# Kernel tuning notes

Measured on AMD Instinct MI355X. Metric: run time of the kernel, lower is better.

## Reference

```python
import jax, jax.numpy as jnp
import numpy as np

# Wrapped Conv2D config (channels_last): input 32x32x32 -> output 32x32x64, 3x3 'same', stride 1
H, W, C_IN, C_OUT = 32, 32, 32, 64


def _propagate(w, b, kernel, bias):
    # w: [B, H*W*C_OUT, n_out], b: [B, n_out]
    B, _, n_out = w.shape
    # transpose(0,2,1) + reshape to [B, n_out, H, W, C_OUT]
    wt = jnp.transpose(w, (0, 2, 1)).reshape(B, n_out, H, W, C_OUT)
    # bias-sum reduction: sum over (h, w, c) of w * bias[c], added to b
    b_new = jnp.einsum('bnhwc,c->bn', wt, bias) + b
    # Batched transposed conv over all n_out slices at once (replaces K.rnn loop)
    z = wt.reshape(B * n_out, H, W, C_OUT)
    w_in = jax.lax.conv_transpose(
        z, kernel, strides=(1, 1), padding='SAME',
        dimension_numbers=('NHWC', 'HWIO', 'NHWC'), transpose_kernel=True)
    # -> [B*n_out, H, W, C_IN]; flatten and transpose back to [B, n_in, n_out]
    w_new = jnp.transpose(w_in.reshape(B, n_out, H * W * C_IN), (0, 2, 1))
    return w_new, b_new


def setup_inputs() -> dict:
    key = jax.random.key(0)
    ks = jax.random.split(key, 6)
    B, n_out = 8, 32
    n_flat = H * W * C_OUT
    return {
        'w_out_u': jax.random.normal(ks[0], (B, n_flat, n_out), jnp.float32),
        'b_out_u': jax.random.normal(ks[1], (B, n_out), jnp.float32),
        'w_out_l': jax.random.normal(ks[2], (B, n_flat, n_out), jnp.float32),
        'b_out_l': jax.random.normal(ks[3], (B, n_out), jnp.float32),
        'kernel': jax.random.normal(ks[4], (3, 3, C_IN, C_OUT), jnp.float32) * 0.1,
        'bias': jax.random.normal(ks[5], (C_OUT,), jnp.float32) * 0.1,
    }


def reference(w_out_u, b_out_u, w_out_l, b_out_l, kernel, bias):
    w_u, b_u = _propagate(w_out_u, b_out_u, kernel, bias)
    w_l, b_l = _propagate(w_out_l, b_out_l, kernel, bias)
    return (w_u, b_u, w_l, b_l)
```

## Files before the change

### kernel.cpp

```cpp
#include <hip/hip_runtime.h>
#include <hip/hip_bf16.h>

#define H  32
#define W  32
#define CI 32
#define CO 64
#define NB 8
#define NOUT 32

#define WU_OFF 0
#define BU_OFF (NB * H * W * CI * NOUT)
#define WL_OFF (BU_OFF + NB * NOUT)
#define BL_OFF (WL_OFF + NB * H * W * CI * NOUT)

#define KF_UINT4 2304
#define BP_OFF_BYTES 36864

typedef __bf16 bf16x8 __attribute__((ext_vector_type(8)));
typedef float  f32x4  __attribute__((ext_vector_type(4)));

__device__ __forceinline__ unsigned int pack_bf16(float lo, float hi) {
    unsigned int ulo = __float_as_uint(lo) + 0x8000u;
    unsigned int uhi = __float_as_uint(hi) + 0x8000u;
    return (uhi & 0xffff0000u) | (ulo >> 16);
}

__global__ void prep_kernel(const float* __restrict__ K,
                            unsigned int* __restrict__ kws,
                            float* __restrict__ bp) {
    int bx = blockIdx.x, t = threadIdx.x;
    if (bx < 9) {
        int g    = bx * 256 + t;
        int tap  = g >> 8;
        int r    = g & 255;
        int i    = r >> 3;
        int og   = r & 7;
        int c    = og >> 2;
        int quad = og & 3;
        int ih   = i >> 4;
        int lane = quad * 16 + (i & 15);
        int dst  = ((tap * 4 + c * 2 + ih) * 64 + lane) * 4;
        const float4* src = (const float4*)(K + (size_t)g * 8);
        float4 f0 = src[0];
        float4 f1 = src[1];
        kws[dst + 0] = pack_bf16(f0.x, f0.y);
        kws[dst + 1] = pack_bf16(f0.z, f0.w);
        kws[dst + 2] = pack_bf16(f1.x, f1.y);
        kws[dst + 3] = pack_bf16(f1.z, f1.w);
    } else {
        bp[(bx - 9) * 256 + t] = 0.f;
    }
}

__global__ __launch_bounds__(512, 4)
void fused_conv_kernel(const float* __restrict__ in0,
                       const float* __restrict__ in1,
                       const uint4* __restrict__ kws,
                       const float* __restrict__ bias,
                       float* __restrict__ bp,
                       float* __restrict__ out0,
                       float* __restrict__ out1) {
    __shared__ uint4 stg[30 * 128];
    __shared__ float bias_s[CO];
    __shared__ float bsum[8][32];

    int t = threadIdx.x;
    if (t < CO) bias_s[t] = bias[t];

    int bx    = blockIdx.x;
    int x     = bx & 7;
    int q     = bx >> 3;
    int combo = x * 2 + (q >> 7);
    int idx   = q & 127;
    int side  = combo >> 3;
    int b     = combo & 7;
    int h     = idx >> 2;
    int wq    = idx & 3;

    const float* inp = (side ? in1 : in0) + (size_t)b * 1024 * 2048;
    const bf16x8* kfp = (const bf16x8*)kws;

    int unit = t >> 5;
    int ogp  = (t >> 3) & 3;
    int n4   = t & 7;
    int wave = t >> 6;
    int lane = t & 63;
    int n16  = lane & 15;
    int quad = lane >> 4;
    int w    = wq * 8 + wave;

    f32x4 acc[2][2] = {};
    float sb[4] = {0.f, 0.f, 0.f, 0.f};
    int rbase = quad * 32 + ((n16 ^ (n16 >> 2)) ^ quad);

    __syncthreads();

    for (int c = 0; c < 2; c++) {
        bf16x8 a[9][2];
#pragma unroll
        for (int tap = 0; tap < 9; tap++) {
            a[tap][0] = kfp[(tap * 4 + c * 2 + 0) * 64 + lane];
            a[tap][1] = kfp[(tap * 4 + c * 2 + 1) * 64 + lane];
        }
#pragma unroll
        for (int s = 0; s < 2; s++) {
            int tile = s * 16 + unit;
            if (tile < 30) {
                int row = tile >= 20 ? 2 : (tile >= 10 ? 1 : 0);
                int col = tile - row * 10;
                int hi  = h - 1 + row;
                int wi  = wq * 8 - 1 + col;
                if (hi >= 0 && hi < H && wi >= 0 && wi < W) {
                    const float* p = inp + (size_t)(hi * W + wi) * 2048
                                   + c * 1024 + ogp * 256 + n4 * 4;
                    float v[8][4];
#pragma unroll
                    for (int j = 0; j < 8; j++) {
                        float4 f = *(const float4*)(p + j * 32);
                        v[j][0] = f.x; v[j][1] = f.y; v[j][2] = f.z; v[j][3] = f.w;
                    }
                    if (row == 1 && col >= 1 && col <= 8) {
#pragma unroll
                        for (int j = 0; j < 8; j++) {
                            float bj = bias_s[c * 32 + ogp * 8 + j];
#pragma unroll
                            for (int k = 0; k < 4; k++)
                                sb[k] = fmaf(v[j][k], bj, sb[k]);
                        }
                    }
                    uint4* dst = &stg[tile * 128 + ogp * 32];
#pragma unroll
                    for (int k = 0; k < 4; k++) {
                        uint4 u;
                        u.x = pack_bf16(v[0][k], v[1][k]);
                        u.y = pack_bf16(v[2][k], v[3][k]);
                        u.z = pack_bf16(v[4][k], v[5][k]);
                        u.w = pack_bf16(v[6][k], v[7][k]);
                        int n = n4 * 4 + k;
                        dst[(n ^ (n >> 2)) ^ ogp] = u;
                    }
                }
            }
        }
        __syncthreads();
        __builtin_amdgcn_s_setprio(1);
#pragma unroll
        for (int kh = 0; kh < 3; kh++) {
            int hi = h + 1 - kh;
            if (hi < 0 || hi >= H) continue;
            int row = 2 - kh;
#pragma unroll
            for (int kw = 0; kw < 3; kw++) {
                int wi = w + 1 - kw;
                if (wi < 0 || wi >= W) continue;
                int col = wave + 2 - kw;
                int tap = kh * 3 + kw;
                const uint4* Tp = &stg[(row * 10 + col) * 128];
                union { uint4 u; bf16x8 v; } b0, b1;
                b0.u = Tp[rbase];
                b1.u = Tp[rbase ^ 20];
                acc[0][0] = __builtin_amdgcn_mfma_f32_16x16x32_bf16(a[tap][0], b0.v, acc[0][0], 0, 0, 0);
                acc[0][1] = __builtin_amdgcn_mfma_f32_16x16x32_bf16(a[tap][0], b1.v, acc[0][1], 0, 0, 0);
                acc[1][0] = __builtin_amdgcn_mfma_f32_16x16x32_bf16(a[tap][1], b0.v, acc[1][0], 0, 0, 0);
                acc[1][1] = __builtin_amdgcn_mfma_f32_16x16x32_bf16(a[tap][1], b1.v, acc[1][1], 0, 0, 0);
            }
        }
        __builtin_amdgcn_s_setprio(0);
        if (c == 0) __syncthreads();
    }

#pragma unroll
    for (int off = 8; off <= 32; off <<= 1)
#pragma unroll
        for (int k = 0; k < 4; k++)
            sb[k] += __shfl_xor(sb[k], off, 64);
    if (lane < 8) {
#pragma unroll
        for (int k = 0; k < 4; k++)
            bsum[wave][lane * 4 + k] = sb[k];
    }
    __syncthreads();
    if (t < 32) {
        float s = 0.f;
#pragma unroll
        for (int wv = 0; wv < 8; wv++) s += bsum[wv][t];
        atomicAdd(&bp[side * 256 + b * 32 + t], s);
    }

    float* outp = (side ? out1 : out0) + (size_t)b * (H * W * CI * NOUT);
    float* wout = outp + (size_t)((h * W + w) * CI) * NOUT;
#pragma unroll
    for (int ih = 0; ih < 2; ih++)
#pragma unroll
        for (int nh = 0; nh < 2; nh++)
#pragma unroll
            for (int r = 0; r < 4; r++) {
                int i = ih * 16 + quad * 4 + r;
                int n = nh * 16 + n16;
                wout[i * NOUT + n] = acc[ih][nh][r];
            }
}

__global__ void bias_final32_kernel(const float* __restrict__ bp,
                                    const float* __restrict__ bu,
                                    const float* __restrict__ bl,
                                    float* __restrict__ out) {
    int sb = blockIdx.x;
    int t  = threadIdx.x;
    if (t >= NOUT) return;
    int side = sb >> 3, b = sb & 7;
    const float* bb = side ? bl : bu;
    out[(side ? BL_OFF : BU_OFF) + b * NOUT + t] =
        bb[b * NOUT + t] + bp[sb * 32 + t];
}

extern "C" void kernel_launch(void* const* d_in, const int* in_sizes, int n_in,
                              void* d_out, int out_size, void* d_ws, size_t ws_size,
                              hipStream_t stream) {
    const float* wu   = (const float*)d_in[0];
    const float* bu   = (const float*)d_in[1];
    const float* wl   = (const float*)d_in[2];
    const float* bl   = (const float*)d_in[3];
    const float* K    = (const float*)d_in[4];
    const float* bias = (const float*)d_in[5];
    float* out = (float*)d_out;
    unsigned int* kws = (unsigned int*)d_ws;
    float* bp = (float*)((char*)d_ws + BP_OFF_BYTES);

    prep_kernel<<<dim3(11), dim3(256), 0, stream>>>(K, kws, bp);
    fused_conv_kernel<<<dim3(2048), dim3(512), 0, stream>>>(
        wu, wl, (const uint4*)d_ws, bias, bp, out + WU_OFF, out + WL_OFF);
    bias_final32_kernel<<<dim3(16), dim3(64), 0, stream>>>(bp, bu, bl, out);
}
```

Measured before the change: 237.8 us.

## Shrink conv blocks to 4 waves, load kernel fragments per tap, disable unrolling

```diff
diff --git a/kernel.cpp b/kernel.cpp
--- a/kernel.cpp
+++ b/kernel.cpp
@@ -52,7 +52,7 @@
     }
 }
 
-__global__ __launch_bounds__(512, 4)
+__global__ __launch_bounds__(256, 4)
 void fused_conv_kernel(const float* __restrict__ in0,
                        const float* __restrict__ in1,
                        const uint4* __restrict__ kws,
@@ -60,9 +60,9 @@
                        float* __restrict__ bp,
                        float* __restrict__ out0,
                        float* __restrict__ out1) {
-    __shared__ uint4 stg[30 * 128];
+    __shared__ uint4 stg[18 * 128];
     __shared__ float bias_s[CO];
-    __shared__ float bsum[8][32];
+    __shared__ float bsum[4][32];
 
     int t = threadIdx.x;
     if (t < CO) bias_s[t] = bias[t];
@@ -70,15 +70,15 @@
     int bx    = blockIdx.x;
     int x     = bx & 7;
     int q     = bx >> 3;
-    int combo = x * 2 + (q >> 7);
-    int idx   = q & 127;
+    int combo = x * 2 + (q >> 8);
+    int inner = q & 255;
     int side  = combo >> 3;
     int b     = combo & 7;
-    int h     = idx >> 2;
-    int wq    = idx & 3;
+    int h     = inner >> 3;
+    int wq4   = inner & 7;
 
     const float* inp = (side ? in1 : in0) + (size_t)b * 1024 * 2048;
-    const bf16x8* kfp = (const bf16x8*)kws;
+    const bf16x8* kfg = (const bf16x8*)kws;
 
     int unit = t >> 5;
     int ogp  = (t >> 3) & 3;
@@ -87,7 +87,7 @@
     int lane = t & 63;
     int n16  = lane & 15;
     int quad = lane >> 4;
-    int w    = wq * 8 + wave;
+    int w    = wq4 * 4 + wave;
 
     f32x4 acc[2][2] = {};
     float sb[4] = {0.f, 0.f, 0.f, 0.f};
@@ -96,20 +96,14 @@
     __syncthreads();
 
     for (int c = 0; c < 2; c++) {
-        bf16x8 a[9][2];
-#pragma unroll
-        for (int tap = 0; tap < 9; tap++) {
-            a[tap][0] = kfp[(tap * 4 + c * 2 + 0) * 64 + lane];
-            a[tap][1] = kfp[(tap * 4 + c * 2 + 1) * 64 + lane];
-        }
-#pragma unroll
-        for (int s = 0; s < 2; s++) {
-            int tile = s * 16 + unit;
-            if (tile < 30) {
-                int row = tile >= 20 ? 2 : (tile >= 10 ? 1 : 0);
-                int col = tile - row * 10;
+#pragma unroll 1
+        for (int s = 0; s < 3; s++) {
+            int tile = s * 8 + unit;
+            if (tile < 18) {
+                int row = tile < 6 ? 0 : (tile < 12 ? 1 : 2);
+                int col = tile - row * 6;
                 int hi  = h - 1 + row;
-                int wi  = wq * 8 - 1 + col;
+                int wi  = wq4 * 4 - 1 + col;
                 if (hi >= 0 && hi < H && wi >= 0 && wi < W) {
                     const float* p = inp + (size_t)(hi * W + wi) * 2048
                                    + c * 1024 + ogp * 256 + n4 * 4;
@@ -119,7 +113,7 @@
                         float4 f = *(const float4*)(p + j * 32);
                         v[j][0] = f.x; v[j][1] = f.y; v[j][2] = f.z; v[j][3] = f.w;
                     }
-                    if (row == 1 && col >= 1 && col <= 8) {
+                    if (row == 1 && col >= 1 && col <= 4) {
 #pragma unroll
                         for (int j = 0; j < 8; j++) {
                             float bj = bias_s[c * 32 + ogp * 8 + j];
@@ -144,25 +138,27 @@
         }
         __syncthreads();
         __builtin_amdgcn_s_setprio(1);
-#pragma unroll
+#pragma unroll 1
         for (int kh = 0; kh < 3; kh++) {
             int hi = h + 1 - kh;
             if (hi < 0 || hi >= H) continue;
             int row = 2 - kh;
-#pragma unroll
+#pragma unroll 1
             for (int kw = 0; kw < 3; kw++) {
                 int wi = w + 1 - kw;
                 if (wi < 0 || wi >= W) continue;
                 int col = wave + 2 - kw;
                 int tap = kh * 3 + kw;
-                const uint4* Tp = &stg[(row * 10 + col) * 128];
+                const uint4* Tp = &stg[(row * 6 + col) * 128];
                 union { uint4 u; bf16x8 v; } b0, b1;
                 b0.u = Tp[rbase];
                 b1.u = Tp[rbase ^ 20];
-                acc[0][0] = __builtin_amdgcn_mfma_f32_16x16x32_bf16(a[tap][0], b0.v, acc[0][0], 0, 0, 0);
-                acc[0][1] = __builtin_amdgcn_mfma_f32_16x16x32_bf16(a[tap][0], b1.v, acc[0][1], 0, 0, 0);
-                acc[1][0] = __builtin_amdgcn_mfma_f32_16x16x32_bf16(a[tap][1], b0.v, acc[1][0], 0, 0, 0);
-                acc[1][1] = __builtin_amdgcn_mfma_f32_16x16x32_bf16(a[tap][1], b1.v, acc[1][1], 0, 0, 0);
+                bf16x8 a0 = kfg[(tap * 4 + c * 2 + 0) * 64 + lane];
+                bf16x8 a1 = kfg[(tap * 4 + c * 2 + 1) * 64 + lane];
+                acc[0][0] = __builtin_amdgcn_mfma_f32_16x16x32_bf16(a0, b0.v, acc[0][0], 0, 0, 0);
+                acc[0][1] = __builtin_amdgcn_mfma_f32_16x16x32_bf16(a0, b1.v, acc[0][1], 0, 0, 0);
+                acc[1][0] = __builtin_amdgcn_mfma_f32_16x16x32_bf16(a1, b0.v, acc[1][0], 0, 0, 0);
+                acc[1][1] = __builtin_amdgcn_mfma_f32_16x16x32_bf16(a1, b1.v, acc[1][1], 0, 0, 0);
             }
         }
         __builtin_amdgcn_s_setprio(0);
@@ -183,7 +179,7 @@
     if (t < 32) {
         float s = 0.f;
 #pragma unroll
-        for (int wv = 0; wv < 8; wv++) s += bsum[wv][t];
+        for (int wv = 0; wv < 4; wv++) s += bsum[wv][t];
         atomicAdd(&bp[side * 256 + b * 32 + t], s);
     }
 
@@ -228,7 +224,7 @@
     float* bp = (float*)((char*)d_ws + BP_OFF_BYTES);
 
     prep_kernel<<<dim3(11), dim3(256), 0, stream>>>(K, kws, bp);
-    fused_conv_kernel<<<dim3(2048), dim3(512), 0, stream>>>(
+    fused_conv_kernel<<<dim3(4096), dim3(256), 0, stream>>>(
         wu, wl, (const uint4*)d_ws, bias, bp, out + WU_OFF, out + WL_OFF);
     bias_final32_kernel<<<dim3(16), dim3(64), 0, stream>>>(bp, bu, bl, out);
 }
```

Result: faster. 218.6 us (-8.1%).
